# Optimization experiments

Hardware: AMD Instinct MI355X
Metric: run time of the kernel (lower is better)

The kernel has to match this reference:

```python
import jax, jax.numpy as jnp
import numpy as np
import math

EPS = 1e-12
SUPPORT = 1  # support_num
NEIGHBOR_NUM = 32

def _l2norm(x, axis):
    n = jnp.sqrt(jnp.sum(x * x, axis=axis, keepdims=True))
    return x / jnp.maximum(n, EPS)

def _sq_dist(a, b):
    # a: (bs, v1, 3), b: (bs, v2, 3) -> (bs, v1, v2)
    inner = jnp.einsum('bic,bjc->bij', a, b)
    a2 = jnp.sum(a * a, axis=-1)
    b2 = jnp.sum(b * b, axis=-1)
    return a2[:, :, None] + b2[:, None, :] - 2.0 * inner

def _knn(verts, k):
    d = _sq_dist(verts, verts)
    _, idx = jax.lax.top_k(-d, k + 1)
    return idx[:, :, 1:]  # drop self

def _gather(t, idx):
    # t: (bs, v, d), idx: (bs, ...) -> (bs, ..., d)
    return jax.vmap(lambda ti, ii: ti[ii])(t, idx)

def _dir_theta(nb_idx, verts, directions):
    nbr = _gather(verts, nb_idx) - verts[:, :, None, :]  # (bs, v, n, 3)
    nbr = _l2norm(nbr, -1)
    sup = _l2norm(directions, 0)  # (3, s*out)
    return jax.nn.relu(jnp.einsum('bvnc,ck->bvnk', nbr, sup))

def _conv_surface(nb_idx, verts, directions, kernel_num):
    theta = _dir_theta(nb_idx, verts, directions)
    bs, v, n, _ = theta.shape
    theta = theta.reshape(bs, v, n, SUPPORT, kernel_num)
    return jnp.sum(jnp.max(theta, axis=2), axis=2)  # (bs, v, kernel)

def _conv_layer(nb_idx, verts, fm, w, b, directions, out_ch):
    theta = _dir_theta(nb_idx, verts, directions)  # (bs, v, n, s*out)
    f = fm @ w + b  # (bs, v, (s+1)*out)
    center = f[..., :out_ch]
    supp_nb = _gather(f[..., out_ch:], nb_idx)  # (bs, v, n, s*out)
    bs, v, n, _ = theta.shape
    act = (theta * supp_nb).reshape(bs, v, n, SUPPORT, out_ch)
    return center + jnp.sum(jnp.max(act, axis=2), axis=2)

def _pool(verts, fm, sample_idx, nbk=4):
    nb = _knn(verts, nbk)
    pooled = jnp.max(_gather(fm, nb), axis=2)
    return verts[:, sample_idx, :], pooled[:, sample_idx, :]

def _nearest(target, source):
    return jnp.argmin(_sq_dist(target, source), axis=-1)  # (bs, v1)

def _forward(vertices, sample_idx1, sample_idx2, dir0, w1, b1, d1, w2, b2, d2,
             w3, b3, d3, w4, b4, d4, cw1, cb1, cw2, cb2, cw3, cb3):
    nb = _knn(vertices, NEIGHBOR_NUM)
    fm_0 = jax.nn.relu(_conv_surface(nb, vertices, dir0, 128))
    fm_1 = jax.nn.relu(_conv_layer(nb, vertices, fm_0, w1, b1, d1, 128))
    v_p1, fm_p1 = _pool(vertices, fm_1, sample_idx1)
    nb = _knn(v_p1, NEIGHBOR_NUM)
    fm_2 = jax.nn.relu(_conv_layer(nb, v_p1, fm_p1, w2, b2, d2, 256))
    fm_3 = jax.nn.relu(_conv_layer(nb, v_p1, fm_2, w3, b3, d3, 256))
    v_p2, fm_p2 = _pool(v_p1, fm_3, sample_idx2)
    nb = _knn(v_p2, NEIGHBOR_NUM)
    fm_4 = _conv_layer(nb, v_p2, fm_p2, w4, b4, d4, 512)  # no relu
    f_global = jnp.max(fm_4, axis=1)  # (bs, 512)
    near1 = _nearest(vertices, v_p1)
    near2 = _nearest(vertices, v_p2)
    fm_2u = _gather(fm_2, near1)
    fm_3u = _gather(fm_3, near1)
    fm_4u = _gather(fm_4, near2)
    bs, v = vertices.shape[0], vertices.shape[1]
    fg = jnp.broadcast_to(f_global[:, None, :], (bs, v, f_global.shape[-1]))
    fuse = jnp.concatenate([fm_0, fm_1, fm_2u, fm_3u, fm_4u, fg], axis=2)  # (bs, v, 1792)
    h = jax.nn.relu(jnp.einsum('bvc,oc->bvo', fuse, cw1) + cb1)
    h = jax.nn.relu(jnp.einsum('bvc,oc->bvo', h, cw2) + cb2)
    return jnp.einsum('bvc,oc->bvo', h, cw3) + cb3  # (bs, v, class_num)


def setup_inputs() -> dict:
    key = jax.random.key(0)
    ks = jax.random.split(key, 24)
    BS, N, CLS = 4, 4096, 13
    def u(k, shape, s):
        return jax.random.uniform(k, shape, jnp.float32, -s, s)
    inp = {}
    inp['vertices'] = jax.random.normal(ks[0], (BS, N, 3), jnp.float32)
    inp['sample_idx1'] = jax.random.permutation(ks[1], N)[:N // 4]
    inp['sample_idx2'] = jax.random.permutation(ks[2], N // 4)[:N // 16]
    inp['dir0'] = u(ks[3], (3, SUPPORT * 128), 1.0 / math.sqrt(SUPPORT * 128))
    def conv_params(k1, k2, k3, cin, cout):
        s = 1.0 / math.sqrt(cout * (SUPPORT + 1))
        return (u(k1, (cin, (SUPPORT + 1) * cout), s),
                u(k2, ((SUPPORT + 1) * cout,), s),
                u(k3, (3, SUPPORT * cout), s))
    inp['w1'], inp['b1'], inp['d1'] = conv_params(ks[4], ks[5], ks[6], 128, 128)
    inp['w2'], inp['b2'], inp['d2'] = conv_params(ks[7], ks[8], ks[9], 128, 256)
    inp['w3'], inp['b3'], inp['d3'] = conv_params(ks[10], ks[11], ks[12], 256, 256)
    inp['w4'], inp['b4'], inp['d4'] = conv_params(ks[13], ks[14], ks[15], 256, 512)
    DF = 1792
    inp['cw1'] = u(ks[16], (512, DF), 1.0 / math.sqrt(DF))
    inp['cb1'] = u(ks[17], (512,), 1.0 / math.sqrt(DF))
    inp['cw2'] = u(ks[18], (512, 512), 1.0 / math.sqrt(512))
    inp['cb2'] = u(ks[19], (512,), 1.0 / math.sqrt(512))
    inp['cw3'] = u(ks[20], (CLS, 512), 1.0 / math.sqrt(512))
    inp['cb3'] = u(ks[21], (CLS,), 1.0 / math.sqrt(512))
    return inp


def reference(vertices, sample_idx1, sample_idx2, dir0, w1, b1, d1, w2, b2, d2,
              w3, b3, d3, w4, b4, d4, cw1, cb1, cw2, cb2, cw3, cb3):
    return _forward(vertices, sample_idx1, sample_idx2, dir0, w1, b1, d1, w2, b2, d2,
                    w3, b3, d3, w4, b4, d4, cw1, cb1, cw2, cb2, cw3, cb3)
```

## Files before the change

kernel.cpp:

```cpp
#include <hip/hip_runtime.h>
#include <cstdint>
#include <cstddef>

namespace {

typedef unsigned short ushort_t;
typedef __bf16 bf16x8 __attribute__((ext_vector_type(8)));
typedef float  f32x4  __attribute__((ext_vector_type(4)));

constexpr int B_ = 4;
constexpr int N0 = 4096;
constexpr int N1 = 1024;
constexpr int N2 = 256;

__device__ __forceinline__ ushort_t f2bf_rne(float x) {
  uint32_t b = __float_as_uint(x);
  b += 0x7FFFu + ((b >> 16) & 1u);
  return (ushort_t)(b >> 16);
}
__device__ __forceinline__ float bf2f(ushort_t h) {
  return __uint_as_float(((uint32_t)h) << 16);
}
__device__ __forceinline__ void split_store(float x, ushort_t* hi, ushort_t* lo,
                                            size_t i) {
  const ushort_t h = f2bf_rne(x);
  hi[i] = h;
  lo[i] = f2bf_rne(x - bf2f(h));
}

__global__ void weight_prep_kernel(
    const float* __restrict__ w1, const float* __restrict__ w2,
    const float* __restrict__ w3, const float* __restrict__ w4,
    const float* __restrict__ cw1, const float* __restrict__ cw2,
    ushort_t* __restrict__ w1th, ushort_t* __restrict__ w1tl,
    ushort_t* __restrict__ w2th, ushort_t* __restrict__ w2tl,
    ushort_t* __restrict__ w3th, ushort_t* __restrict__ w3tl,
    ushort_t* __restrict__ w4th, ushort_t* __restrict__ w4tl,
    ushort_t* __restrict__ w1h, ushort_t* __restrict__ w1l,
    ushort_t* __restrict__ w2h, ushort_t* __restrict__ w2l)
{
  const int i = blockIdx.x * blockDim.x + threadIdx.x;
  if (i < 32768) {
    const int j = i, k = j % 128, n = j / 128;
    split_store(w1[(size_t)k * 256 + n], w1th, w1tl, (size_t)n * 128 + k);
  } else if (i < 98304) {
    const int j = i - 32768, k = j % 128, n = j / 128;
    split_store(w2[(size_t)k * 512 + n], w2th, w2tl, (size_t)n * 128 + k);
  } else if (i < 229376) {
    const int j = i - 98304, k = j % 256, n = j / 256;
    split_store(w3[(size_t)k * 512 + n], w3th, w3tl, (size_t)n * 256 + k);
  } else if (i < 491520) {
    const int j = i - 229376, k = j % 256, n = j / 256;
    split_store(w4[(size_t)k * 1024 + n], w4th, w4tl, (size_t)n * 256 + k);
  } else if (i < 1409024) {
    const int j = i - 491520;
    split_store(cw1[j], w1h, w1l, j);
  } else if (i < 1671168) {
    const int j = i - 1409024;
    split_store(cw2[j], w2h, w2l, j);
  }
}

__device__ __forceinline__ void bitonic_sort64(float& sd, int& si, int lane) {
#pragma unroll
  for (int kk = 2; kk <= 64; kk <<= 1) {
#pragma unroll
    for (int j = kk >> 1; j > 0; j >>= 1) {
      const float od = __shfl_xor(sd, j);
      const int   oi = __shfl_xor(si, j);
      const bool less    = (sd < od) || (sd == od && si < oi);
      const bool wantMin = ((lane & j) == 0) == ((lane & kk) == 0);
      if (wantMin != less) { sd = od; si = oi; }
    }
  }
}

__device__ __forceinline__ void knn_flush(float& ld, int& li, float& tau,
                                          int cnt, const float* bufd,
                                          const int* bufi, int lane, int Km1) {
  float sd = (lane < cnt) ? bufd[lane] : INFINITY;
  int   si = (lane < cnt) ? bufi[lane] : 0x7fffffff;
  bitonic_sort64(sd, si, lane);
  const float rd = __shfl(sd, 63 - lane);
  const int   ri = __shfl(si, 63 - lane);
  const bool keep = (ld < rd) || (ld == rd && li < ri);
  float md = keep ? ld : rd;
  int   mi = keep ? li : ri;
#pragma unroll
  for (int j = 32; j > 0; j >>= 1) {
    const float od = __shfl_xor(md, j);
    const int   oi = __shfl_xor(mi, j);
    const bool less    = (md < od) || (md == od && mi < oi);
    const bool wantMin = ((lane & j) == 0);
    if (wantMin != less) { md = od; mi = oi; }
  }
  ld = md; li = mi;
  tau = __shfl(ld, Km1);
}

template<int K, int TILE>
__launch_bounds__(1024)
__global__ void knn_wave_kernel(const float* __restrict__ pts,
                                int Q, int C,
                                int* __restrict__ out)
{
  __shared__ float4 sp[TILE];
  __shared__ float sbd[16][64];
  __shared__ int   sbi[16][64];
  const int b    = blockIdx.y;
  const int lane = threadIdx.x & 63;
  const int wid  = threadIdx.x >> 6;
  const int q    = blockIdx.x * 16 + wid;
  const int self = q;
  const float* pb = pts + (size_t)b * C * 3;
  const float qx = pb[self * 3 + 0];
  const float qy = pb[self * 3 + 1];
  const float qz = pb[self * 3 + 2];
  const float q2   = qx * qx + qy * qy + qz * qz;
  const float m2qx = -2.0f * qx, m2qy = -2.0f * qy, m2qz = -2.0f * qz;

  float ld = INFINITY; int li = 0x7fffffff;
  float tau = INFINITY;
  int cnt = 0;
  float* bufd = sbd[wid];
  int*   bufi = sbi[wid];

  auto append = [&](unsigned long long m, bool cand, float d, int ci) {
    const int c = __popcll(m);
    if (cnt + c > 64) {
      knn_flush(ld, li, tau, cnt, bufd, bufi, lane, K - 1);
      cnt = 0;
    }
    const int prefix = __popcll(m & ((1ull << lane) - 1ull));
    if (cand) { bufd[cnt + prefix] = d; bufi[cnt + prefix] = ci; }
    cnt += c;
  };

  for (int t0 = 0; t0 < C; t0 += TILE) {
    __syncthreads();
    for (int i = threadIdx.x; i < TILE; i += 1024) {
      const float x = pb[(t0 + i) * 3 + 0];
      const float y = pb[(t0 + i) * 3 + 1];
      const float z = pb[(t0 + i) * 3 + 2];
      sp[i] = make_float4(x, y, z, x * x + y * y + z * z);
    }
    __syncthreads();
    int base = 0;
    if (t0 == 0) {
      const float4 p = sp[lane];
      const float d = fmaf(m2qx, p.x, fmaf(m2qy, p.y, fmaf(m2qz, p.z, p.w + q2)));
      const bool valid = (lane != self);
      float sd = valid ? d : INFINITY;
      int   si = valid ? lane : 0x7fffffff;
      bitonic_sort64(sd, si, lane);
      ld = sd; li = si;
      tau = __shfl(ld, K - 1);
      base = 64;
    }
    for (; base + 128 <= TILE; base += 128) {
      const int ci0 = t0 + base + lane;
      const int ci1 = ci0 + 64;
      const float4 p0 = sp[base + lane];
      const float4 p1 = sp[base + 64 + lane];
      const float d0 = fmaf(m2qx, p0.x, fmaf(m2qy, p0.y, fmaf(m2qz, p0.z, p0.w + q2)));
      const float d1 = fmaf(m2qx, p1.x, fmaf(m2qy, p1.y, fmaf(m2qz, p1.z, p1.w + q2)));
      const bool c0 = (ci0 != self) && (d0 < tau);
      const bool c1 = (ci1 != self) && (d1 < tau);
      const unsigned long long m0 = __ballot(c0);
      const unsigned long long m1 = __ballot(c1);
      if (m0) append(m0, c0, d0, ci0);
      if (m1) append(m1, c1, d1, ci1);
    }
    if (base < TILE) {
      const int ci = t0 + base + lane;
      const float4 p = sp[base + lane];
      const float d = fmaf(m2qx, p.x, fmaf(m2qy, p.y, fmaf(m2qz, p.z, p.w + q2)));
      const bool c = (ci != self) && (d < tau);
      const unsigned long long m = __ballot(c);
      if (m) append(m, c, d, ci);
    }
  }
  if (cnt > 0) knn_flush(ld, li, tau, cnt, bufd, bufi, lane, K - 1);
  if (lane < K) out[((size_t)b * Q + q) * K + lane] = li;
}

__launch_bounds__(256)
__global__ void nearest_dual_kernel(const float* __restrict__ qpts,
                                    const float* __restrict__ cpts1,
                                    const float* __restrict__ cpts2,
                                    int* __restrict__ out1,
                                    int* __restrict__ out2)
{
  __shared__ float4 sp[1024];
  const int lvl = blockIdx.y;
  const int C = lvl ? N2 : N1;
  const float* cpts = lvl ? cpts2 : cpts1;
  int* out = lvl ? out2 : out1;
  const int lane = threadIdx.x & 63;
  const int wid  = threadIdx.x >> 6;
  const int q    = blockIdx.x * 4 + wid;
  const int b    = q >> 12;
  const float qx = qpts[(size_t)q * 3 + 0];
  const float qy = qpts[(size_t)q * 3 + 1];
  const float qz = qpts[(size_t)q * 3 + 2];
  const float q2   = qx * qx + qy * qy + qz * qz;
  const float m2qx = -2.0f * qx, m2qy = -2.0f * qy, m2qz = -2.0f * qz;
  const float* pb = cpts + (size_t)b * C * 3;

  for (int i = threadIdx.x; i < C; i += 256) {
    const float x = pb[i * 3 + 0];
    const float y = pb[i * 3 + 1];
    const float z = pb[i * 3 + 2];
    sp[i] = make_float4(x, y, z, x * x + y * y + z * z);
  }
  __syncthreads();
  float best = INFINITY; int bi = 0x7fffffff;
  for (int base = 0; base < C; base += 64) {
    const float4 p = sp[base + lane];
    const float d = fmaf(m2qx, p.x, fmaf(m2qy, p.y, fmaf(m2qz, p.z, p.w + q2)));
    if (d < best) { best = d; bi = base + lane; }
  }
#pragma unroll
  for (int j = 1; j < 64; j <<= 1) {
    const float od = __shfl_xor(best, j);
    const int   oi = __shfl_xor(bi, j);
    if (od < best || (od == best && oi < bi)) { best = od; bi = oi; }
  }
  if (lane == 0) out[q] = bi;
}

__global__ void conv_surface_kernel(const float* __restrict__ verts,
                                    const int*   __restrict__ nb,
                                    const float* __restrict__ dir,
                                    int V, int C,
                                    ushort_t* __restrict__ outH,
                                    ushort_t* __restrict__ outL) {
  __shared__ float ux[32], uy[32], uz[32];
  const int bv = blockIdx.x;
  const int b = bv / V;
  const int v = bv - b * V;
  const float* vb = verts + (size_t)b * V * 3;
  if (threadIdx.x < 32) {
    const float cx = vb[v * 3 + 0], cy = vb[v * 3 + 1], cz = vb[v * 3 + 2];
    const int nidx = nb[(size_t)bv * 32 + threadIdx.x];
    const float dx = vb[nidx * 3 + 0] - cx;
    const float dy = vb[nidx * 3 + 1] - cy;
    const float dz = vb[nidx * 3 + 2] - cz;
    const float rn = 1.0f / fmaxf(sqrtf(dx * dx + dy * dy + dz * dz), 1e-12f);
    ux[threadIdx.x] = dx * rn; uy[threadIdx.x] = dy * rn; uz[threadIdx.x] = dz * rn;
  }
  __syncthreads();
  const int o = threadIdx.x;
  float d0 = dir[o], d1 = dir[C + o], d2 = dir[2 * C + o];
  const float rn = 1.0f / fmaxf(sqrtf(d0 * d0 + d1 * d1 + d2 * d2), 1e-12f);
  d0 *= rn; d1 *= rn; d2 *= rn;
  float m = -INFINITY;
#pragma unroll
  for (int n = 0; n < 32; ++n) {
    const float t = fmaxf(0.0f, fmaf(d2, uz[n], fmaf(d1, uy[n], d0 * ux[n])));
    m = fmaxf(m, t);
  }
  split_store(fmaxf(0.0f, m), outH, outL, (size_t)bv * C + o);
}

__global__ void conv_combine_kernel(const float* __restrict__ f,
                                    const int*   __restrict__ nb,
                                    const float* __restrict__ dir,
                                    const float* __restrict__ verts,
                                    int V, int C, int relu,
                                    ushort_t* __restrict__ outH,
                                    ushort_t* __restrict__ outL) {
  __shared__ float ux[32], uy[32], uz[32];
  __shared__ int snb[32];
  const int bv = blockIdx.x;
  const int b = bv / V;
  const int v = bv - b * V;
  const float* vb = verts + (size_t)b * V * 3;
  if (threadIdx.x < 32) {
    const float cx = vb[v * 3 + 0], cy = vb[v * 3 + 1], cz = vb[v * 3 + 2];
    const int nidx = nb[(size_t)bv * 32 + threadIdx.x];
    snb[threadIdx.x] = nidx;
    const float dx = vb[nidx * 3 + 0] - cx;
    const float dy = vb[nidx * 3 + 1] - cy;
    const float dz = vb[nidx * 3 + 2] - cz;
    const float rn = 1.0f / fmaxf(sqrtf(dx * dx + dy * dy + dz * dz), 1e-12f);
    ux[threadIdx.x] = dx * rn; uy[threadIdx.x] = dy * rn; uz[threadIdx.x] = dz * rn;
  }
  __syncthreads();
  const int o = threadIdx.x;
  float d0 = dir[o], d1 = dir[C + o], d2 = dir[2 * C + o];
  const float rn = 1.0f / fmaxf(sqrtf(d0 * d0 + d1 * d1 + d2 * d2), 1e-12f);
  d0 *= rn; d1 *= rn; d2 *= rn;
  const float* fb = f + (size_t)b * V * 2 * C;
  float m = -INFINITY;
#pragma unroll 8
  for (int n = 0; n < 32; ++n) {
    const float t = fmaxf(0.0f, fmaf(d2, uz[n], fmaf(d1, uy[n], d0 * ux[n])));
    const float s = fb[(size_t)snb[n] * 2 * C + C + o];
    m = fmaxf(m, t * s);
  }
  float r = fb[(size_t)v * 2 * C + o] + m;
  if (relu) r = fmaxf(r, 0.0f);
  split_store(r, outH, outL, (size_t)bv * C + o);
}

__global__ void pool_kernel(const ushort_t* __restrict__ fmH,
                            const ushort_t* __restrict__ fmL,
                            const int*   __restrict__ nb,
                            const int*   __restrict__ sidx,
                            int Q, int Vsrc, int C,
                            ushort_t* __restrict__ outH,
                            ushort_t* __restrict__ outL) {
  const int i = blockIdx.x * blockDim.x + threadIdx.x;
  if (i >= B_ * Q * C) return;
  const int c = i % C;
  const int q = (i / C) % Q;
  const int b = i / (C * Q);
  const int* nn = nb + ((size_t)b * Vsrc + sidx[q]) * 32;
  const size_t fb = (size_t)b * Vsrc * C;
  float m = -INFINITY;
#pragma unroll
  for (int t = 0; t < 4; ++t) {
    const size_t idx = fb + (size_t)nn[t] * C + c;
    m = fmaxf(m, bf2f(fmH[idx]) + bf2f(fmL[idx]));
  }
  split_store(m, outH, outL, (size_t)i);
}

__global__ void gather_verts_kernel(const float* __restrict__ src,
                                    const int* __restrict__ idx,
                                    int Vsrc, int Q, float* __restrict__ dst) {
  const int i = blockIdx.x * blockDim.x + threadIdx.x;
  if (i >= B_ * Q * 3) return;
  const int c = i % 3;
  const int q = (i / 3) % Q;
  const int b = i / (3 * Q);
  dst[i] = src[((size_t)b * Vsrc + idx[q]) * 3 + c];
}

__global__ void global_max_kernel(const ushort_t* __restrict__ fmH,
                                  const ushort_t* __restrict__ fmL,
                                  ushort_t* __restrict__ outH,
                                  ushort_t* __restrict__ outL) {
  __shared__ float red[4][64];
  const int t = threadIdx.x;
  const int cl = t & 63, slice = t >> 6;
  const int c = (blockIdx.x & 7) * 64 + cl;
  const int b = blockIdx.x >> 3;
  const size_t base = (size_t)b * 256 * 512 + c;
  float m = -INFINITY;
  for (int v = slice; v < 256; v += 4) {
    const size_t idx = base + (size_t)v * 512;
    m = fmaxf(m, bf2f(fmH[idx]) + bf2f(fmL[idx]));
  }
  red[slice][cl] = m;
  __syncthreads();
  if (slice == 0) {
    m = fmaxf(fmaxf(red[0][cl], red[1][cl]), fmaxf(red[2][cl], red[3][cl]));
    split_store(m, outH, outL, (size_t)b * 512 + c);
  }
}

constexpr int LDT = 40;

template<bool FUSE, bool SPLITOUT, bool RELU>
__launch_bounds__(256)
__global__ void mfma_gemm_kernel(
    const ushort_t* __restrict__ Ahi, const ushort_t* __restrict__ Alo,
    const ushort_t* __restrict__ f0h, const ushort_t* __restrict__ f0l,
    const ushort_t* __restrict__ f1h, const ushort_t* __restrict__ f1l,
    const ushort_t* __restrict__ f2h, const ushort_t* __restrict__ f2l,
    const ushort_t* __restrict__ f3h, const ushort_t* __restrict__ f3l,
    const ushort_t* __restrict__ f4h, const ushort_t* __restrict__ f4l,
    const ushort_t* __restrict__ fgh, const ushort_t* __restrict__ fgl,
    const int* __restrict__ near1, const int* __restrict__ near2,
    const ushort_t* __restrict__ Bhi, const ushort_t* __restrict__ Blo,
    const float* __restrict__ bias, int K,
    float* __restrict__ outF, ushort_t* __restrict__ outHi,
    ushort_t* __restrict__ outLo, int Nn)
{
  __shared__ ushort_t As_h[128 * LDT];
  __shared__ ushort_t As_l[128 * LDT];
  __shared__ ushort_t Bs_h[128 * LDT];
  __shared__ ushort_t Bs_l[128 * LDT];

  const int tid  = threadIdx.x;
  const int lane = tid & 63;
  const int wv   = tid >> 6;
  const int wr   = wv >> 1, wc = wv & 1;
  const int quad = lane >> 4, ml = lane & 15;
  const int m0 = blockIdx.y * 128, n0 = blockIdx.x * 128;

  const int r  = tid >> 1;
  const int hh = (tid & 1) * 16;

  int fb = 0, r1 = 0, r2 = 0;
  if (FUSE) {
    const int m = m0 + r;
    fb = m >> 12;
    r1 = near1[m];
    r2 = near2[m];
  }

  f32x4 acc[4][4];
#pragma unroll
  for (int i = 0; i < 4; ++i)
#pragma unroll
    for (int j = 0; j < 4; ++j) acc[i][j] = f32x4{0.f, 0.f, 0.f, 0.f};

  for (int k0 = 0; k0 < K; k0 += 32) {
    const int k = k0 + hh;
    uint4 a0h, a1h, a0l, a1l;
    {
      const ushort_t *sh, *sl; size_t off;
      if (FUSE) {
        const int m = m0 + r;
        if (k < 128)       { sh = f0h; sl = f0l; off = (size_t)m * 128 + k; }
        else if (k < 256)  { sh = f1h; sl = f1l; off = (size_t)m * 128 + (k - 128); }
        else if (k < 512)  { sh = f2h; sl = f2l; off = ((size_t)fb * 1024 + r1) * 256 + (k - 256); }
        else if (k < 768)  { sh = f3h; sl = f3l; off = ((size_t)fb * 1024 + r1) * 256 + (k - 512); }
        else if (k < 1280) { sh = f4h; sl = f4l; off = ((size_t)fb * 256 + r2) * 512 + (k - 768); }
        else               { sh = fgh; sl = fgl; off = (size_t)fb * 512 + (k - 1280); }
      } else {
        sh = Ahi; sl = Alo; off = (size_t)(m0 + r) * K + k;
      }
      a0h = *(const uint4*)(sh + off); a1h = *(const uint4*)(sh + off + 8);
      a0l = *(const uint4*)(sl + off); a1l = *(const uint4*)(sl + off + 8);
    }
    uint4 b0h, b1h, b0l, b1l;
    {
      const size_t off = (size_t)(n0 + r) * K + k;
      b0h = *(const uint4*)(Bhi + off); b1h = *(const uint4*)(Bhi + off + 8);
      b0l = *(const uint4*)(Blo + off); b1l = *(const uint4*)(Blo + off + 8);
    }
    __syncthreads();
    *(uint4*)&As_h[r * LDT + hh]     = a0h;
    *(uint4*)&As_h[r * LDT + hh + 8] = a1h;
    *(uint4*)&As_l[r * LDT + hh]     = a0l;
    *(uint4*)&As_l[r * LDT + hh + 8] = a1l;
    *(uint4*)&Bs_h[r * LDT + hh]     = b0h;
    *(uint4*)&Bs_h[r * LDT + hh + 8] = b1h;
    *(uint4*)&Bs_l[r * LDT + hh]     = b0l;
    *(uint4*)&Bs_l[r * LDT + hh + 8] = b1l;
    __syncthreads();

    bf16x8 ah[4], al[4], bh[4], bl[4];
#pragma unroll
    for (int i = 0; i < 4; ++i) {
      const int row = wr * 64 + i * 16 + ml;
      ah[i] = *(const bf16x8*)&As_h[row * LDT + quad * 8];
      al[i] = *(const bf16x8*)&As_l[row * LDT + quad * 8];
    }
#pragma unroll
    for (int j = 0; j < 4; ++j) {
      const int row = wc * 64 + j * 16 + ml;
      bh[j] = *(const bf16x8*)&Bs_h[row * LDT + quad * 8];
      bl[j] = *(const bf16x8*)&Bs_l[row * LDT + quad * 8];
    }
#pragma unroll
    for (int i = 0; i < 4; ++i)
#pragma unroll
      for (int j = 0; j < 4; ++j) {
        acc[i][j] = __builtin_amdgcn_mfma_f32_16x16x32_bf16(al[i], bh[j], acc[i][j], 0, 0, 0);
        acc[i][j] = __builtin_amdgcn_mfma_f32_16x16x32_bf16(ah[i], bl[j], acc[i][j], 0, 0, 0);
        acc[i][j] = __builtin_amdgcn_mfma_f32_16x16x32_bf16(ah[i], bh[j], acc[i][j], 0, 0, 0);
      }
  }

#pragma unroll
  for (int i = 0; i < 4; ++i)
#pragma unroll
    for (int j = 0; j < 4; ++j) {
      const int n = n0 + wc * 64 + j * 16 + ml;
      const float bv = bias[n];
#pragma unroll
      for (int reg = 0; reg < 4; ++reg) {
        const int m = m0 + wr * 64 + i * 16 + quad * 4 + reg;
        float r = acc[i][j][reg] + bv;
        if (RELU) r = fmaxf(r, 0.0f);
        if (SPLITOUT) {
          const ushort_t h = f2bf_rne(r);
          outHi[(size_t)m * Nn + n] = h;
          outLo[(size_t)m * Nn + n] = f2bf_rne(r - bf2f(h));
        } else {
          outF[(size_t)m * Nn + n] = r;
        }
      }
    }
}

__global__ void head_kernel(const float* __restrict__ h,
                            const float* __restrict__ cw,
                            const float* __restrict__ cb,
                            float* __restrict__ out) {
  const int i = blockIdx.x * blockDim.x + threadIdx.x;
  if (i >= B_ * N0 * 13) return;
  const int o = i % 13;
  const int row = i / 13;
  const float4* hr = (const float4*)(h + (size_t)row * 512);
  const float4* wr = (const float4*)(cw + (size_t)o * 512);
  float acc = cb[o];
  for (int k = 0; k < 128; ++k) {
    const float4 a = hr[k], w = wr[k];
    acc = fmaf(a.x, w.x, fmaf(a.y, w.y, fmaf(a.z, w.z, fmaf(a.w, w.w, acc))));
  }
  out[i] = acc;
}

}

extern "C" void kernel_launch(void* const* d_in, const int* in_sizes, int n_in,
                              void* d_out, int out_size, void* d_ws, size_t ws_size,
                              hipStream_t stream)
{
  const float* vertices = (const float*)d_in[0];
  const int*   sidx1    = (const int*)  d_in[1];
  const int*   sidx2    = (const int*)  d_in[2];
  const float* dir0     = (const float*)d_in[3];
  const float* w1 = (const float*)d_in[4];
  const float* b1 = (const float*)d_in[5];
  const float* d1 = (const float*)d_in[6];
  const float* w2 = (const float*)d_in[7];
  const float* b2 = (const float*)d_in[8];
  const float* d2 = (const float*)d_in[9];
  const float* w3 = (const float*)d_in[10];
  const float* b3 = (const float*)d_in[11];
  const float* d3 = (const float*)d_in[12];
  const float* w4 = (const float*)d_in[13];
  const float* b4 = (const float*)d_in[14];
  const float* d4 = (const float*)d_in[15];
  const float* cw1 = (const float*)d_in[16];
  const float* cb1 = (const float*)d_in[17];
  const float* cw2 = (const float*)d_in[18];
  const float* cb2 = (const float*)d_in[19];
  const float* cw3 = (const float*)d_in[20];
  const float* cb3 = (const float*)d_in[21];
  (void)in_sizes; (void)n_in; (void)out_size; (void)ws_size;

  char* ws = (char*)d_ws;
  size_t off = 0;
  auto alloc = [&](size_t bytes) -> void* {
    void* p = ws + off;
    off += (bytes + 255) & ~(size_t)255;
    return p;
  };

  int*   nb1   = (int*)  alloc((size_t)B_ * N0 * 32 * 4);
  int*   nb2   = (int*)  alloc((size_t)B_ * N1 * 32 * 4);
  int*   nb3   = (int*)  alloc((size_t)B_ * N2 * 32 * 4);
  float* vp1   = (float*)alloc((size_t)B_ * N1 * 3 * 4);
  float* vp2   = (float*)alloc((size_t)B_ * N2 * 3 * 4);
  int*   near1 = (int*)  alloc((size_t)B_ * N0 * 4);
  int*   near2 = (int*)  alloc((size_t)B_ * N0 * 4);
  float* h2    = (float*)alloc((size_t)B_ * N0 * 512 * 4);
  float* fbuf  = (float*)alloc((size_t)B_ * N0 * 256 * 4);

  const size_t nF0 = (size_t)B_ * N0 * 128;
  const size_t nP1 = (size_t)B_ * N1 * 128;
  const size_t nF2 = (size_t)B_ * N1 * 256;
  const size_t nP2 = (size_t)B_ * N2 * 256;
  const size_t nF4 = (size_t)B_ * N2 * 512;
  const size_t nFg = (size_t)B_ * 512;
  const size_t nW1 = (size_t)512 * 1792;
  const size_t nW2 = (size_t)512 * 512;
  const size_t nH1 = (size_t)B_ * N0 * 512;
  ushort_t* f0h = (ushort_t*)alloc(nF0 * 2); ushort_t* f0l = (ushort_t*)alloc(nF0 * 2);
  ushort_t* f1h = (ushort_t*)alloc(nF0 * 2); ushort_t* f1l = (ushort_t*)alloc(nF0 * 2);
  ushort_t* p1h = (ushort_t*)alloc(nP1 * 2); ushort_t* p1l = (ushort_t*)alloc(nP1 * 2);
  ushort_t* f2h = (ushort_t*)alloc(nF2 * 2); ushort_t* f2l = (ushort_t*)alloc(nF2 * 2);
  ushort_t* f3h = (ushort_t*)alloc(nF2 * 2); ushort_t* f3l = (ushort_t*)alloc(nF2 * 2);
  ushort_t* p2h = (ushort_t*)alloc(nP2 * 2); ushort_t* p2l = (ushort_t*)alloc(nP2 * 2);
  ushort_t* f4h = (ushort_t*)alloc(nF4 * 2); ushort_t* f4l = (ushort_t*)alloc(nF4 * 2);
  ushort_t* fgh = (ushort_t*)alloc(nFg * 2); ushort_t* fgl = (ushort_t*)alloc(nFg * 2);
  ushort_t* w1h = (ushort_t*)alloc(nW1 * 2); ushort_t* w1l = (ushort_t*)alloc(nW1 * 2);
  ushort_t* w2h = (ushort_t*)alloc(nW2 * 2); ushort_t* w2l = (ushort_t*)alloc(nW2 * 2);
  ushort_t* h1h = (ushort_t*)alloc(nH1 * 2); ushort_t* h1l = (ushort_t*)alloc(nH1 * 2);
  ushort_t* w1th = (ushort_t*)alloc((size_t)256 * 128 * 2);
  ushort_t* w1tl = (ushort_t*)alloc((size_t)256 * 128 * 2);
  ushort_t* w2th = (ushort_t*)alloc((size_t)512 * 128 * 2);
  ushort_t* w2tl = (ushort_t*)alloc((size_t)512 * 128 * 2);
  ushort_t* w3th = (ushort_t*)alloc((size_t)512 * 256 * 2);
  ushort_t* w3tl = (ushort_t*)alloc((size_t)512 * 256 * 2);
  ushort_t* w4th = (ushort_t*)alloc((size_t)1024 * 256 * 2);
  ushort_t* w4tl = (ushort_t*)alloc((size_t)1024 * 256 * 2);

  const dim3 blk256(256), blk1024(1024);
  auto mgemm = [&](const ushort_t* Ah, const ushort_t* Al,
                   const ushort_t* Bh, const ushort_t* Bl, const float* bias,
                   int M, int Nn, int K, float* outF) {
    const dim3 grid(Nn / 128, M / 128);
    mfma_gemm_kernel<false, false, false><<<grid, blk256, 0, stream>>>(
        Ah, Al, nullptr, nullptr, nullptr, nullptr, nullptr, nullptr, nullptr,
        nullptr, nullptr, nullptr, nullptr, nullptr, nullptr, nullptr,
        Bh, Bl, bias, K, outF, nullptr, nullptr, Nn);
  };

  weight_prep_kernel<<<dim3(6528), blk256, 0, stream>>>(
      w1, w2, w3, w4, cw1, cw2,
      w1th, w1tl, w2th, w2tl, w3th, w3tl, w4th, w4tl,
      w1h, w1l, w2h, w2l);

  knn_wave_kernel<32, 2048><<<dim3(N0 / 16, B_), blk1024, 0, stream>>>(vertices, N0, N0, nb1);
  conv_surface_kernel<<<dim3(B_ * N0), dim3(128), 0, stream>>>(
      vertices, nb1, dir0, N0, 128, f0h, f0l);
  mgemm(f0h, f0l, w1th, w1tl, b1, B_ * N0, 256, 128, fbuf);
  conv_combine_kernel<<<dim3(B_ * N0), dim3(128), 0, stream>>>(
      fbuf, nb1, d1, vertices, N0, 128, 1, f1h, f1l);

  gather_verts_kernel<<<dim3((B_ * N1 * 3 + 255) / 256), blk256, 0, stream>>>(vertices, sidx1, N0, N1, vp1);
  pool_kernel<<<dim3((B_ * N1 * 128 + 255) / 256), blk256, 0, stream>>>(
      f1h, f1l, nb1, sidx1, N1, N0, 128, p1h, p1l);

  knn_wave_kernel<32, 1024><<<dim3(N1 / 16, B_), blk1024, 0, stream>>>(vp1, N1, N1, nb2);
  mgemm(p1h, p1l, w2th, w2tl, b2, B_ * N1, 512, 128, fbuf);
  conv_combine_kernel<<<dim3(B_ * N1), dim3(256), 0, stream>>>(
      fbuf, nb2, d2, vp1, N1, 256, 1, f2h, f2l);
  mgemm(f2h, f2l, w3th, w3tl, b3, B_ * N1, 512, 256, fbuf);
  conv_combine_kernel<<<dim3(B_ * N1), dim3(256), 0, stream>>>(
      fbuf, nb2, d3, vp1, N1, 256, 1, f3h, f3l);

  gather_verts_kernel<<<dim3((B_ * N2 * 3 + 255) / 256), blk256, 0, stream>>>(vp1, sidx2, N1, N2, vp2);
  pool_kernel<<<dim3((B_ * N2 * 256 + 255) / 256), blk256, 0, stream>>>(
      f3h, f3l, nb2, sidx2, N2, N1, 256, p2h, p2l);

  knn_wave_kernel<32, 256><<<dim3(N2 / 16, B_), blk1024, 0, stream>>>(vp2, N2, N2, nb3);
  mgemm(p2h, p2l, w4th, w4tl, b4, B_ * N2, 1024, 256, fbuf);
  conv_combine_kernel<<<dim3(B_ * N2), dim3(512), 0, stream>>>(
      fbuf, nb3, d4, vp2, N2, 512, 0, f4h, f4l);
  global_max_kernel<<<dim3(B_ * 8), blk256, 0, stream>>>(f4h, f4l, fgh, fgl);

  nearest_dual_kernel<<<dim3((B_ * N0) / 4, 2), blk256, 0, stream>>>(
      vertices, vp1, vp2, near1, near2);

  mfma_gemm_kernel<true, true, true><<<dim3(512 / 128, (B_ * N0) / 128), blk256, 0, stream>>>(
      nullptr, nullptr,
      f0h, f0l, f1h, f1l, f2h, f2l, f3h, f3l, f4h, f4l, fgh, fgl,
      near1, near2, w1h, w1l, cb1, 1792, nullptr, h1h, h1l, 512);
  mfma_gemm_kernel<false, false, true><<<dim3(512 / 128, (B_ * N0) / 128), blk256, 0, stream>>>(
      h1h, h1l,
      nullptr, nullptr, nullptr, nullptr, nullptr, nullptr, nullptr, nullptr,
      nullptr, nullptr, nullptr, nullptr,
      nullptr, nullptr, w2h, w2l, cb2, 512, h2, nullptr, nullptr, 512);
  head_kernel<<<dim3((B_ * N0 * 13 + 255) / 256), blk256, 0, stream>>>(h2, cw3, cb3, (float*)d_out);
}
```

Measured before the change: 666.5 us.

## Merge three KNN launches into one kernel and fold vertex gathers into prep

Moves the sampled-vertex gathers into the weight prep kernel, which now computes vp2 straight from the original vertices through both index arrays. Because all point sets exist up front, the three KNN passes become one launch of 512-thread blocks that picks its level from the block index, so the small levels can overlap with the big one. The head layer is rewritten so one wave handles a row, with the weights staged in shared memory and a shuffle reduction across lanes. This cuts launch count and serialization between dependent kernels. In exchange, blocks are smaller and work per block is uneven across the three levels.

Measured after the change: 580.2 us. 13.0% less time.

```diff
diff --git a/kernel.cpp b/kernel.cpp
--- a/kernel.cpp
+++ b/kernel.cpp
@@ -28,16 +28,19 @@
   lo[i] = f2bf_rne(x - bf2f(h));
 }
 
-__global__ void weight_prep_kernel(
+__global__ void prep_kernel(
     const float* __restrict__ w1, const float* __restrict__ w2,
     const float* __restrict__ w3, const float* __restrict__ w4,
     const float* __restrict__ cw1, const float* __restrict__ cw2,
+    const float* __restrict__ vertices,
+    const int* __restrict__ sidx1, const int* __restrict__ sidx2,
     ushort_t* __restrict__ w1th, ushort_t* __restrict__ w1tl,
     ushort_t* __restrict__ w2th, ushort_t* __restrict__ w2tl,
     ushort_t* __restrict__ w3th, ushort_t* __restrict__ w3tl,
     ushort_t* __restrict__ w4th, ushort_t* __restrict__ w4tl,
     ushort_t* __restrict__ w1h, ushort_t* __restrict__ w1l,
-    ushort_t* __restrict__ w2h, ushort_t* __restrict__ w2l)
+    ushort_t* __restrict__ w2h, ushort_t* __restrict__ w2l,
+    float* __restrict__ vp1, float* __restrict__ vp2)
 {
   const int i = blockIdx.x * blockDim.x + threadIdx.x;
   if (i < 32768) {
@@ -58,6 +61,14 @@
   } else if (i < 1671168) {
     const int j = i - 1409024;
     split_store(cw2[j], w2h, w2l, j);
+  } else if (i < 1683456) {
+    const int j = i - 1671168;
+    const int c = j % 3, q = (j / 3) % N1, b = j / (3 * N1);
+    vp1[j] = vertices[((size_t)b * N0 + sidx1[q]) * 3 + c];
+  } else if (i < 1686528) {
+    const int j = i - 1683456;
+    const int c = j % 3, q = (j / 3) % N2, b = j / (3 * N2);
+    vp2[j] = vertices[((size_t)b * N0 + sidx1[sidx2[q]]) * 3 + c];
   }
 }
 
@@ -98,19 +109,29 @@
   tau = __shfl(ld, Km1);
 }
 
-template<int K, int TILE>
-__launch_bounds__(1024)
-__global__ void knn_wave_kernel(const float* __restrict__ pts,
-                                int Q, int C,
-                                int* __restrict__ out)
+__launch_bounds__(512)
+__global__ void knn_mega_kernel(const float* __restrict__ verts,
+                                const float* __restrict__ vp1,
+                                const float* __restrict__ vp2,
+                                int* __restrict__ nb1,
+                                int* __restrict__ nb2,
+                                int* __restrict__ nb3)
 {
+  constexpr int K = 32, TILE = 2048;
   __shared__ float4 sp[TILE];
-  __shared__ float sbd[16][64];
-  __shared__ int   sbi[16][64];
-  const int b    = blockIdx.y;
+  __shared__ float sbd[8][64];
+  __shared__ int   sbi[8][64];
+
+  int bx = blockIdx.x;
+  const float* pts; int Q, C; int* out;
+  if (bx < 2048)      { pts = verts; Q = N0; C = N0; out = nb1; }
+  else if (bx < 2560) { pts = vp1;   Q = N1; C = N1; out = nb2; bx -= 2048; }
+  else                { pts = vp2;   Q = N2; C = N2; out = nb3; bx -= 2560; }
+  const int bpb = Q / 8;
+  const int b  = bx / bpb;
   const int lane = threadIdx.x & 63;
   const int wid  = threadIdx.x >> 6;
-  const int q    = blockIdx.x * 16 + wid;
+  const int q    = (bx % bpb) * 8 + wid;
   const int self = q;
   const float* pb = pts + (size_t)b * C * 3;
   const float qx = pb[self * 3 + 0];
@@ -137,8 +158,9 @@
   };
 
   for (int t0 = 0; t0 < C; t0 += TILE) {
+    const int nt = (C - t0 < TILE) ? (C - t0) : TILE;
     __syncthreads();
-    for (int i = threadIdx.x; i < TILE; i += 1024) {
+    for (int i = threadIdx.x; i < nt; i += 512) {
       const float x = pb[(t0 + i) * 3 + 0];
       const float y = pb[(t0 + i) * 3 + 1];
       const float z = pb[(t0 + i) * 3 + 2];
@@ -157,7 +179,7 @@
       tau = __shfl(ld, K - 1);
       base = 64;
     }
-    for (; base + 128 <= TILE; base += 128) {
+    for (; base + 128 <= nt; base += 128) {
       const int ci0 = t0 + base + lane;
       const int ci1 = ci0 + 64;
       const float4 p0 = sp[base + lane];
@@ -171,7 +193,7 @@
       if (m0) append(m0, c0, d0, ci0);
       if (m1) append(m1, c1, d1, ci1);
     }
-    if (base < TILE) {
+    if (base < nt) {
       const int ci = t0 + base + lane;
       const float4 p = sp[base + lane];
       const float d = fmaf(m2qx, p.x, fmaf(m2qy, p.y, fmaf(m2qz, p.z, p.w + q2)));
@@ -327,17 +349,6 @@
   split_store(m, outH, outL, (size_t)i);
 }
 
-__global__ void gather_verts_kernel(const float* __restrict__ src,
-                                    const int* __restrict__ idx,
-                                    int Vsrc, int Q, float* __restrict__ dst) {
-  const int i = blockIdx.x * blockDim.x + threadIdx.x;
-  if (i >= B_ * Q * 3) return;
-  const int c = i % 3;
-  const int q = (i / 3) % Q;
-  const int b = i / (3 * Q);
-  dst[i] = src[((size_t)b * Vsrc + idx[q]) * 3 + c];
-}
-
 __global__ void global_max_kernel(const ushort_t* __restrict__ fmH,
                                   const ushort_t* __restrict__ fmL,
                                   ushort_t* __restrict__ outH,
@@ -489,22 +500,31 @@
     }
 }
 
-__global__ void head_kernel(const float* __restrict__ h,
-                            const float* __restrict__ cw,
-                            const float* __restrict__ cb,
-                            float* __restrict__ out) {
-  const int i = blockIdx.x * blockDim.x + threadIdx.x;
-  if (i >= B_ * N0 * 13) return;
-  const int o = i % 13;
-  const int row = i / 13;
+__launch_bounds__(256)
+__global__ void head_wave_kernel(const float* __restrict__ h,
+                                 const float* __restrict__ cw,
+                                 const float* __restrict__ cb,
+                                 float* __restrict__ out) {
+  __shared__ float ws[13 * 512];
+  __shared__ float cbs[13];
+  const int lane = threadIdx.x & 63;
+  const int wid  = threadIdx.x >> 6;
+  for (int i = threadIdx.x; i < 13 * 512; i += 256) ws[i] = cw[i];
+  if (threadIdx.x < 13) cbs[threadIdx.x] = cb[threadIdx.x];
+  __syncthreads();
+  const int row = blockIdx.x * 4 + wid;
   const float4* hr = (const float4*)(h + (size_t)row * 512);
-  const float4* wr = (const float4*)(cw + (size_t)o * 512);
-  float acc = cb[o];
-  for (int k = 0; k < 128; ++k) {
-    const float4 a = hr[k], w = wr[k];
-    acc = fmaf(a.x, w.x, fmaf(a.y, w.y, fmaf(a.z, w.z, fmaf(a.w, w.w, acc))));
-  }
-  out[i] = acc;
+  const float4 a0 = hr[lane * 2], a1 = hr[lane * 2 + 1];
+#pragma unroll
+  for (int o = 0; o < 13; ++o) {
+    const float4* wr = (const float4*)(ws + o * 512);
+    const float4 w0 = wr[lane * 2], w1 = wr[lane * 2 + 1];
+    float p = a0.x * w0.x + a0.y * w0.y + a0.z * w0.z + a0.w * w0.w
+            + a1.x * w1.x + a1.y * w1.y + a1.z * w1.z + a1.w * w1.w;
+#pragma unroll
+    for (int j = 1; j < 64; j <<= 1) p += __shfl_xor(p, j);
+    if (lane == 0) out[(size_t)row * 13 + o] = p + cbs[o];
+  }
 }
 
 }
@@ -584,7 +604,7 @@
   ushort_t* w4th = (ushort_t*)alloc((size_t)1024 * 256 * 2);
   ushort_t* w4tl = (ushort_t*)alloc((size_t)1024 * 256 * 2);
 
-  const dim3 blk256(256), blk1024(1024);
+  const dim3 blk256(256), blk512(512);
   auto mgemm = [&](const ushort_t* Ah, const ushort_t* Al,
                    const ushort_t* Bh, const ushort_t* Bl, const float* bias,
                    int M, int Nn, int K, float* outF) {
@@ -595,23 +615,23 @@
         Bh, Bl, bias, K, outF, nullptr, nullptr, Nn);
   };
 
-  weight_prep_kernel<<<dim3(6528), blk256, 0, stream>>>(
-      w1, w2, w3, w4, cw1, cw2,
+  prep_kernel<<<dim3(6588), blk256, 0, stream>>>(
+      w1, w2, w3, w4, cw1, cw2, vertices, sidx1, sidx2,
       w1th, w1tl, w2th, w2tl, w3th, w3tl, w4th, w4tl,
-      w1h, w1l, w2h, w2l);
-
-  knn_wave_kernel<32, 2048><<<dim3(N0 / 16, B_), blk1024, 0, stream>>>(vertices, N0, N0, nb1);
+      w1h, w1l, w2h, w2l, vp1, vp2);
+
+  knn_mega_kernel<<<dim3(2688), blk512, 0, stream>>>(
+      vertices, vp1, vp2, nb1, nb2, nb3);
+
   conv_surface_kernel<<<dim3(B_ * N0), dim3(128), 0, stream>>>(
       vertices, nb1, dir0, N0, 128, f0h, f0l);
   mgemm(f0h, f0l, w1th, w1tl, b1, B_ * N0, 256, 128, fbuf);
   conv_combine_kernel<<<dim3(B_ * N0), dim3(128), 0, stream>>>(
       fbuf, nb1, d1, vertices, N0, 128, 1, f1h, f1l);
 
-  gather_verts_kernel<<<dim3((B_ * N1 * 3 + 255) / 256), blk256, 0, stream>>>(vertices, sidx1, N0, N1, vp1);
   pool_kernel<<<dim3((B_ * N1 * 128 + 255) / 256), blk256, 0, stream>>>(
       f1h, f1l, nb1, sidx1, N1, N0, 128, p1h, p1l);
 
-  knn_wave_kernel<32, 1024><<<dim3(N1 / 16, B_), blk1024, 0, stream>>>(vp1, N1, N1, nb2);
   mgemm(p1h, p1l, w2th, w2tl, b2, B_ * N1, 512, 128, fbuf);
   conv_combine_kernel<<<dim3(B_ * N1), dim3(256), 0, stream>>>(
       fbuf, nb2, d2, vp1, N1, 256, 1, f2h, f2l);
@@ -619,11 +639,9 @@
   conv_combine_kernel<<<dim3(B_ * N1), dim3(256), 0, stream>>>(
       fbuf, nb2, d3, vp1, N1, 256, 1, f3h, f3l);
 
-  gather_verts_kernel<<<dim3((B_ * N2 * 3 + 255) / 256), blk256, 0, stream>>>(vp1, sidx2, N1, N2, vp2);
   pool_kernel<<<dim3((B_ * N2 * 256 + 255) / 256), blk256, 0, stream>>>(
       f3h, f3l, nb2, sidx2, N2, N1, 256, p2h, p2l);
 
-  knn_wave_kernel<32, 256><<<dim3(N2 / 16, B_), blk1024, 0, stream>>>(vp2, N2, N2, nb3);
   mgemm(p2h, p2l, w4th, w4tl, b4, B_ * N2, 1024, 256, fbuf);
   conv_combine_kernel<<<dim3(B_ * N2), dim3(512), 0, stream>>>(
       fbuf, nb3, d4, vp2, N2, 512, 0, f4h, f4l);
@@ -641,5 +659,6 @@
       nullptr, nullptr, nullptr, nullptr, nullptr, nullptr, nullptr, nullptr,
       nullptr, nullptr, nullptr, nullptr,
       nullptr, nullptr, w2h, w2l, cb2, 512, h2, nullptr, nullptr, 512);
-  head_kernel<<<dim3((B_ * N0 * 13 + 255) / 256), blk256, 0, stream>>>(h2, cw3, cb3, (float*)d_out);
-}
+  head_wave_kernel<<<dim3((B_ * N0) / 4), blk256, 0, stream>>>(
+      h2, cw3, cb3, (float*)d_out);
+}
```
